# Kernel optimization log

Hardware: AMD Instinct MI355X
Metric: run time of the kernel (lower is better)

## Reference

```python
import jax, jax.numpy as jnp
import numpy as np

D_MODEL = 768
N_HEADS = 12
D_K = D_MODEL // N_HEADS
B, S = 2, 4096


def setup_inputs() -> dict:
    key = jax.random.key(0)
    ks = jax.random.split(key, 12)
    s_in = 1.0 / np.sqrt(D_MODEL)
    inp = {
        "Q": jax.random.normal(ks[0], (B, S, D_MODEL), jnp.float32),
        "K": jax.random.normal(ks[1], (B, S, D_MODEL), jnp.float32),
        "V": jax.random.normal(ks[2], (B, S, D_MODEL), jnp.float32),
        # nn.Linear weights are [out, in]; applied as x @ W.T + b
        "Wq": jax.random.normal(ks[3], (D_MODEL, D_MODEL), jnp.float32) * s_in,
        "bq": jax.random.normal(ks[4], (D_MODEL,), jnp.float32) * s_in,
        "Wk": jax.random.normal(ks[5], (D_MODEL, D_MODEL), jnp.float32) * s_in,
        "bk": jax.random.normal(ks[6], (D_MODEL,), jnp.float32) * s_in,
        "Wv": jax.random.normal(ks[7], (D_MODEL, D_MODEL), jnp.float32) * s_in,
        "bv": jax.random.normal(ks[8], (D_MODEL,), jnp.float32) * s_in,
        "Wo": jax.random.normal(ks[9], (D_MODEL, D_MODEL), jnp.float32) * s_in,
        "bo": jax.random.normal(ks[10], (D_MODEL,), jnp.float32) * s_in,
    }
    return inp


def _split_heads(x):
    b, s, _ = x.shape
    return x.reshape(b, s, N_HEADS, D_K).transpose(0, 2, 1, 3)  # [b,h,s,dk]


def reference(Q, K, V, Wq, bq, Wk, bk, Wv, bv, Wo, bo):
    q = _split_heads(Q @ Wq.T + bq)
    k = _split_heads(K @ Wk.T + bk)
    v = _split_heads(V @ Wv.T + bv)
    scale = 1.0 / np.sqrt(D_K).astype(np.float32)
    scores = jnp.einsum("bhqd,bhkd->bhqk", q, k) * scale  # [B,H,S,S]
    attn = jax.nn.softmax(scores, axis=-1)
    out = jnp.einsum("bhqk,bhkd->bhqd", attn, v)
    out = out.transpose(0, 2, 1, 3).reshape(Q.shape[0], Q.shape[1], D_MODEL)
    return out @ Wo.T + bo
```

## Files before the change

kernel.cpp:

```cpp
#include <hip/hip_runtime.h>
#include <hip/hip_bf16.h>

typedef __attribute__((ext_vector_type(8))) short short8;
typedef __attribute__((ext_vector_type(4))) float f32x4;
typedef __attribute__((ext_vector_type(4))) unsigned short ushort4v;

static __device__ __forceinline__ unsigned short f2bf(float f) {
  unsigned u = __float_as_uint(f);
  unsigned r = (u + 0x7fffu + ((u >> 16) & 1u)) >> 16;
  return (unsigned short)r;
}
static __device__ __forceinline__ short8 pack8(float4 a, float4 b) {
  short8 r;
  r[0] = (short)f2bf(a.x); r[1] = (short)f2bf(a.y);
  r[2] = (short)f2bf(a.z); r[3] = (short)f2bf(a.w);
  r[4] = (short)f2bf(b.x); r[5] = (short)f2bf(b.y);
  r[6] = (short)f2bf(b.z); r[7] = (short)f2bf(b.w);
  return r;
}

template <int CTRL>
static __device__ __forceinline__ float fmax_dpp(float x) {
  int t = __builtin_amdgcn_update_dpp(__float_as_int(x), __float_as_int(x),
                                      CTRL, 0xF, 0xF, true);
  return fmaxf(x, __int_as_float(t));
}
static __device__ __forceinline__ float max16_dpp(float x) {
  x = fmax_dpp<0xB1>(x);
  x = fmax_dpp<0x4E>(x);
  x = fmax_dpp<0x141>(x);
  x = fmax_dpp<0x140>(x);
  return x;
}

template<int XF32, int OUTF32>
__device__ __forceinline__ void gemm128(
    const void* Xp, const float* W, const float* bias,
    void* outp, float scale, int vt_mode, int bm, int bn)
{
  __shared__ unsigned short Als[128 * 32];
  __shared__ unsigned short Bls[128 * 32];

  const int tid = threadIdx.x;
  const int wave = tid >> 6, lane = tid & 63;
  const int g = lane >> 4, lo = lane & 15;
  const int wr = wave >> 1, wc = wave & 1;
  const int m0 = bm * 128, n0 = bn * 128;

  const f32x4 vzero = {0.f, 0.f, 0.f, 0.f};
  f32x4 acc[4][4];
#pragma unroll
  for (int m = 0; m < 4; ++m)
#pragma unroll
    for (int n = 0; n < 4; ++n) acc[m][n] = vzero;

  const int arow = tid >> 1;
  const int acol = (tid & 1) * 16;
  const float* Af = nullptr;
  const unsigned short* Ab = nullptr;
  if constexpr (XF32) Af = (const float*)Xp + (size_t)(m0 + arow) * 768 + acol;
  else                Ab = (const unsigned short*)Xp + (size_t)(m0 + arow) * 768 + acol;
  const float* Brow = W + (size_t)(n0 + arow) * 768 + acol;

  for (int k0 = 0; k0 < 768; k0 += 32) {
    short8 va0, va1;
    if constexpr (XF32) {
      float4 f0 = *(const float4*)(Af + k0);
      float4 f1 = *(const float4*)(Af + k0 + 4);
      float4 f2 = *(const float4*)(Af + k0 + 8);
      float4 f3 = *(const float4*)(Af + k0 + 12);
      va0 = pack8(f0, f1);
      va1 = pack8(f2, f3);
    } else {
      va0 = *(const short8*)(Ab + k0);
      va1 = *(const short8*)(Ab + k0 + 8);
    }
    float4 g0 = *(const float4*)(Brow + k0);
    float4 g1 = *(const float4*)(Brow + k0 + 4);
    float4 g2 = *(const float4*)(Brow + k0 + 8);
    float4 g3 = *(const float4*)(Brow + k0 + 12);
    short8 vb0 = pack8(g0, g1);
    short8 vb1 = pack8(g2, g3);

    __syncthreads();
    *(short8*)(Als + arow * 32 + acol)     = va0;
    *(short8*)(Als + arow * 32 + acol + 8) = va1;
    *(short8*)(Bls + arow * 32 + acol)     = vb0;
    *(short8*)(Bls + arow * 32 + acol + 8) = vb1;
    __syncthreads();

    short8 af[4], bf[4];
#pragma unroll
    for (int m = 0; m < 4; ++m)
      af[m] = *(const short8*)(Als + (wr * 64 + m * 16 + lo) * 32 + g * 8);
#pragma unroll
    for (int n = 0; n < 4; ++n)
      bf[n] = *(const short8*)(Bls + (wc * 64 + n * 16 + lo) * 32 + g * 8);
#pragma unroll
    for (int m = 0; m < 4; ++m)
#pragma unroll
      for (int n = 0; n < 4; ++n)
        acc[m][n] = __builtin_amdgcn_mfma_f32_16x16x32_bf16(af[m], bf[n], acc[m][n], 0, 0, 0);
  }

#pragma unroll
  for (int n = 0; n < 4; ++n) {
    const int ncol = n0 + wc * 64 + n * 16 + lo;
    const float bb = bias[ncol];
#pragma unroll
    for (int m = 0; m < 4; ++m) {
      const int rowb = m0 + wr * 64 + m * 16 + g * 4;
      if constexpr (OUTF32) {
        float* out = (float*)outp;
#pragma unroll
        for (int r = 0; r < 4; ++r)
          out[(size_t)(rowb + r) * 768 + ncol] = (acc[m][n][r] + bb) * scale;
      } else {
        unsigned short* out = (unsigned short*)outp;
        if (!vt_mode) {
#pragma unroll
          for (int r = 0; r < 4; ++r)
            out[(size_t)(rowb + r) * 768 + ncol] = f2bf((acc[m][n][r] + bb) * scale);
        } else {
          const int b = rowb >> 12, s = rowb & 4095;
          const int hh = ncol >> 6, d = ncol & 63;
          ushort4v pk;
#pragma unroll
          for (int r = 0; r < 4; ++r) pk[r] = f2bf((acc[m][n][r] + bb) * scale);
          *(ushort4v*)(out + (((size_t)b * 12 + hh) * 64 + d) * 4096 + s) = pk;
        }
      }
    }
  }
}

__global__ __launch_bounds__(256, 2) void qkv_proj(
    const float* __restrict__ Qi, const float* __restrict__ Ki,
    const float* __restrict__ Vi,
    const float* __restrict__ Wq, const float* __restrict__ bq,
    const float* __restrict__ Wk, const float* __restrict__ bk,
    const float* __restrict__ Wv, const float* __restrict__ bv,
    unsigned short* __restrict__ qo, unsigned short* __restrict__ ko,
    unsigned short* __restrict__ vto)
{
  const int z = blockIdx.z;
  const float* X = (z == 0) ? Qi : (z == 1) ? Ki : Vi;
  const float* W = (z == 0) ? Wq : (z == 1) ? Wk : Wv;
  const float* bb = (z == 0) ? bq : (z == 1) ? bk : bv;
  unsigned short* out = (z == 0) ? qo : (z == 1) ? ko : vto;
  const float scale = (z == 0) ? 0.18033688011f : 1.0f;
  gemm128<1, 0>(X, W, bb, out, scale, (z == 2) ? 1 : 0, blockIdx.x, blockIdx.y);
}

__global__ __launch_bounds__(256, 2) void out_proj(
    const unsigned short* __restrict__ X, const float* __restrict__ W,
    const float* __restrict__ bias, float* __restrict__ out)
{
  gemm128<0, 1>(X, W, bias, out, 1.0f, 0, blockIdx.x, blockIdx.y);
}

__global__ __launch_bounds__(512, 4) void attn_fwd(
    const unsigned short* qw, const unsigned short* __restrict__ kw,
    const unsigned short* __restrict__ vtw, unsigned short* ow)
{
  __shared__ char LDS[34816];

  const int tid = threadIdx.x, wave = tid >> 6, lane = tid & 63;
  const int g = lane >> 4, lo = lane & 15;
  const int bh = blockIdx.y, b = bh / 12, hh = bh % 12;
  const int q0 = blockIdx.x * 128 + wave * 16;

  short8 aq[2];
#pragma unroll
  for (int s = 0; s < 2; ++s)
    aq[s] = *(const short8*)(qw + (size_t)(b * 4096 + q0 + lo) * 768
                             + hh * 64 + s * 32 + g * 8);

  const f32x4 vzero = {0.f, 0.f, 0.f, 0.f};
  float mx[4];
  f32x4 lacc = vzero;
  f32x4 oacc[4];
#pragma unroll
  for (int r = 0; r < 4; ++r) mx[r] = -1e30f;
#pragma unroll
  for (int n = 0; n < 4; ++n) oacc[n] = vzero;

  short8 bone;
#pragma unroll
  for (int j = 0; j < 8; ++j) bone[j] = (short)0x3F80;

  const int rsw = (lo & 7) << 4;
  const int rb0 = lo * 128 + ((g * 16) ^ rsw);
  const int rb1 = lo * 128 + ((64 + g * 16) ^ rsw);
  char* const Kr0 = LDS + rb0;
  char* const Kr1 = LDS + rb1;
  char* const Vr0 = LDS + 8192 + rb0;
  char* const Vr1 = LDS + 8192 + rb1;
  char* const Pwr = LDS + 16384 + wave * 2304 + (g * 4) * 144 + lo * 2;
  char* const Prd = LDS + 16384 + wave * 2304 + lo * 144 + g * 16;

  const int srow = tid >> 3;
  const int sc = tid & 7;
  const unsigned short* krow = kw + ((size_t)b * 4096 + srow) * 768 + hh * 64 + sc * 8;
  const unsigned short* vrow = vtw + ((size_t)bh * 64 + srow) * 4096 + sc * 8;
  const int sdst = srow * 128 + ((sc * 16) ^ ((srow & 7) << 4));
  char* const Ksd = LDS + sdst;
  char* const Vsd = LDS + 8192 + sdst;

  short8 kl = *(const short8*)(krow);
  short8 vl = *(const short8*)(vrow);

  for (int kv0 = 0; kv0 < 4096; kv0 += 64) {
    asm volatile("s_waitcnt lgkmcnt(0)" ::: "memory");
    __builtin_amdgcn_s_barrier();
    *(short8*)Ksd = kl;
    *(short8*)Vsd = vl;
    if (kv0 + 64 < 4096) {
      kl = *(const short8*)(krow + (size_t)(kv0 + 64) * 768);
      vl = *(const short8*)(vrow + (kv0 + 64));
    }
    asm volatile("s_waitcnt lgkmcnt(0)" ::: "memory");
    __builtin_amdgcn_s_barrier();
    __builtin_amdgcn_sched_barrier(0);

    f32x4 sa[4];
#pragma unroll
    for (int n = 0; n < 4; ++n) {
      short8 bk0 = *(const short8*)(Kr0 + n * 2048);
      short8 bk1 = *(const short8*)(Kr1 + n * 2048);
      f32x4 t = vzero;
      t = __builtin_amdgcn_mfma_f32_16x16x32_bf16(aq[0], bk0, t, 0, 0, 0);
      t = __builtin_amdgcn_mfma_f32_16x16x32_bf16(aq[1], bk1, t, 0, 0, 0);
      sa[n] = t;
    }

#pragma unroll
    for (int r = 0; r < 4; ++r) {
      float pm = fmaxf(fmaxf(sa[0][r], sa[1][r]), fmaxf(sa[2][r], sa[3][r]));
      pm = max16_dpp(pm);
      if (pm > mx[r] + 8.f) {
        const float fr = __builtin_amdgcn_exp2f(mx[r] - pm);
        mx[r] = pm;
        lacc[r] *= fr;
#pragma unroll
        for (int nd = 0; nd < 4; ++nd) oacc[nd][r] *= fr;
      }
#pragma unroll
      for (int n = 0; n < 4; ++n) {
        const float pv = __builtin_amdgcn_exp2f(sa[n][r] - mx[r]);
        *(unsigned short*)(Pwr + r * 144 + n * 32) =
            (unsigned short)(__float_as_uint(pv) >> 16);
      }
    }

    short8 ap0 = *(const short8*)(Prd);
    short8 ap1 = *(const short8*)(Prd + 64);
#pragma unroll
    for (int nd = 0; nd < 4; ++nd) {
      short8 bv0 = *(const short8*)(Vr0 + nd * 2048);
      short8 bv1 = *(const short8*)(Vr1 + nd * 2048);
      oacc[nd] = __builtin_amdgcn_mfma_f32_16x16x32_bf16(ap0, bv0, oacc[nd], 0, 0, 0);
      oacc[nd] = __builtin_amdgcn_mfma_f32_16x16x32_bf16(ap1, bv1, oacc[nd], 0, 0, 0);
    }
    lacc = __builtin_amdgcn_mfma_f32_16x16x32_bf16(ap0, bone, lacc, 0, 0, 0);
    lacc = __builtin_amdgcn_mfma_f32_16x16x32_bf16(ap1, bone, lacc, 0, 0, 0);
  }

#pragma unroll
  for (int r = 0; r < 4; ++r) {
    const float inv = 1.f / lacc[r];
    const size_t rowoff = (size_t)(b * 4096 + q0 + g * 4 + r) * 768 + hh * 64;
#pragma unroll
    for (int nd = 0; nd < 4; ++nd)
      ow[rowoff + nd * 16 + lo] = f2bf(oacc[nd][r] * inv);
  }
}

extern "C" void kernel_launch(void* const* d_in, const int* in_sizes, int n_in,
                              void* d_out, int out_size, void* d_ws, size_t ws_size,
                              hipStream_t stream) {
  (void)in_sizes; (void)n_in; (void)out_size; (void)ws_size;
  const float* Qi = (const float*)d_in[0];
  const float* Ki = (const float*)d_in[1];
  const float* Vi = (const float*)d_in[2];
  const float* Wq = (const float*)d_in[3];
  const float* bq = (const float*)d_in[4];
  const float* Wk = (const float*)d_in[5];
  const float* bk = (const float*)d_in[6];
  const float* Wv = (const float*)d_in[7];
  const float* bv = (const float*)d_in[8];
  const float* Wo = (const float*)d_in[9];
  const float* bo = (const float*)d_in[10];

  unsigned short* ws = (unsigned short*)d_ws;
  const size_t NTOK = 8192u * 768u;
  unsigned short* qw  = ws;
  unsigned short* vtw = ws + NTOK;
  unsigned short* kwp = (unsigned short*)d_out;

  qkv_proj<<<dim3(64, 6, 3), 256, 0, stream>>>(Qi, Ki, Vi, Wq, bq, Wk, bk,
                                               Wv, bv, qw, kwp, vtw);
  attn_fwd<<<dim3(32, 24, 1), 512, 0, stream>>>(qw, kwp, vtw, qw);
  out_proj<<<dim3(64, 6, 1), 256, 0, stream>>>(qw, Wo, bo, (float*)d_out);
}
```

Baseline: 296.7 us.

## Double-buffer K/V tiles in LDS with one barrier per attention tile

The attention loop now keeps two K/V tile buffers in LDS. While the QK^T MFMAs run on one buffer, the next tile (already fetched into registers) is stored into the other, and loads for the tile after that are issued. This replaces two barriers per tile with one and lets global loads overlap more compute. In exchange it raises LDS use from about 34KB to 50KB per block, which may reduce occupancy, and past the end it issues clamped redundant loads of the last tile.

```diff
diff --git a/kernel.cpp b/kernel.cpp
--- a/kernel.cpp
+++ b/kernel.cpp
@@ -159,11 +159,69 @@
   gemm128<0, 1>(X, W, bias, out, 1.0f, 0, blockIdx.x, blockIdx.y);
 }
 
+#define ATTN_TILE(BO, KWR, VWR, KLD, VLD, TNEXT)                               \
+  {                                                                            \
+    asm volatile("s_waitcnt lgkmcnt(0)" ::: "memory");                         \
+    __builtin_amdgcn_s_barrier();                                              \
+    __builtin_amdgcn_sched_barrier(0);                                         \
+                                                    \
+    f32x4 sa[4];                                                               \
+    _Pragma("unroll")                                                          \
+    for (int n = 0; n < 4; ++n) {                                              \
+      short8 bk0 = *(const short8*)(Kr0 + (BO) + n * 2048);                    \
+      short8 bk1 = *(const short8*)(Kr1 + (BO) + n * 2048);                    \
+      f32x4 t = vzero;                                                         \
+      t = __builtin_amdgcn_mfma_f32_16x16x32_bf16(aq[0], bk0, t, 0, 0, 0);     \
+      t = __builtin_amdgcn_mfma_f32_16x16x32_bf16(aq[1], bk1, t, 0, 0, 0);     \
+      sa[n] = t;                                                               \
+    }                                                                          \
+             \
+    *(short8*)(Ksd + ((BO) ^ 8192)) = KWR;                                     \
+    *(short8*)(Vsd + ((BO) ^ 8192)) = VWR;                                     \
+    {                                                                          \
+      int tp = (TNEXT);                                                        \
+      if (tp > 63) tp = 63;                                                    \
+      KLD = *(const short8*)(krow + (size_t)(tp * 64) * 768);                  \
+      VLD = *(const short8*)(vrow + tp * 64);                                  \
+    }                                                                          \
+                                                 \
+    _Pragma("unroll")                                                          \
+    for (int r = 0; r < 4; ++r) {                                              \
+      float pm = fmaxf(fmaxf(sa[0][r], sa[1][r]), fmaxf(sa[2][r], sa[3][r]));  \
+      pm = max16_dpp(pm);                                                      \
+      if (pm > mx[r] + 8.f) {                                                  \
+        const float fr = __builtin_amdgcn_exp2f(mx[r] - pm);                   \
+        mx[r] = pm;                                                            \
+        lacc[r] *= fr;                                                         \
+        _Pragma("unroll")                                                      \
+        for (int nd = 0; nd < 4; ++nd) oacc[nd][r] *= fr;                      \
+      }                                                                        \
+      _Pragma("unroll")                                                        \
+      for (int n = 0; n < 4; ++n) {                                            \
+        const float pv = __builtin_amdgcn_exp2f(sa[n][r] - mx[r]);             \
+        *(unsigned short*)(Pwr + r * 144 + n * 32) =                           \
+            (unsigned short)(__float_as_uint(pv) >> 16);                       \
+      }                                                                        \
+    }                                                                          \
+                                        \
+    short8 ap0 = *(const short8*)(Prd);                                        \
+    short8 ap1 = *(const short8*)(Prd + 64);                                   \
+    _Pragma("unroll")                                                          \
+    for (int nd = 0; nd < 4; ++nd) {                                           \
+      short8 bv0 = *(const short8*)(Vr0 + (BO) + nd * 2048);                   \
+      short8 bv1 = *(const short8*)(Vr1 + (BO) + nd * 2048);                   \
+      oacc[nd] = __builtin_amdgcn_mfma_f32_16x16x32_bf16(ap0, bv0, oacc[nd], 0, 0, 0); \
+      oacc[nd] = __builtin_amdgcn_mfma_f32_16x16x32_bf16(ap1, bv1, oacc[nd], 0, 0, 0); \
+    }                                                                          \
+    lacc = __builtin_amdgcn_mfma_f32_16x16x32_bf16(ap0, bone, lacc, 0, 0, 0);  \
+    lacc = __builtin_amdgcn_mfma_f32_16x16x32_bf16(ap1, bone, lacc, 0, 0, 0);  \
+  }
+
 __global__ __launch_bounds__(512, 4) void attn_fwd(
     const unsigned short* qw, const unsigned short* __restrict__ kw,
     const unsigned short* __restrict__ vtw, unsigned short* ow)
 {
-  __shared__ char LDS[34816];
+  __shared__ char LDS[51200];
 
   const int tid = threadIdx.x, wave = tid >> 6, lane = tid & 63;
   const int g = lane >> 4, lo = lane & 15;
@@ -194,10 +252,10 @@
   const int rb1 = lo * 128 + ((64 + g * 16) ^ rsw);
   char* const Kr0 = LDS + rb0;
   char* const Kr1 = LDS + rb1;
-  char* const Vr0 = LDS + 8192 + rb0;
-  char* const Vr1 = LDS + 8192 + rb1;
-  char* const Pwr = LDS + 16384 + wave * 2304 + (g * 4) * 144 + lo * 2;
-  char* const Prd = LDS + 16384 + wave * 2304 + lo * 144 + g * 16;
+  char* const Vr0 = LDS + 16384 + rb0;
+  char* const Vr1 = LDS + 16384 + rb1;
+  char* const Pwr = LDS + 32768 + wave * 2304 + (g * 4) * 144 + lo * 2;
+  char* const Prd = LDS + 32768 + wave * 2304 + lo * 144 + g * 16;
 
   const int srow = tid >> 3;
   const int sc = tid & 7;
@@ -205,65 +263,21 @@
   const unsigned short* vrow = vtw + ((size_t)bh * 64 + srow) * 4096 + sc * 8;
   const int sdst = srow * 128 + ((sc * 16) ^ ((srow & 7) << 4));
   char* const Ksd = LDS + sdst;
-  char* const Vsd = LDS + 8192 + sdst;
-
-  short8 kl = *(const short8*)(krow);
-  short8 vl = *(const short8*)(vrow);
-
-  for (int kv0 = 0; kv0 < 4096; kv0 += 64) {
-    asm volatile("s_waitcnt lgkmcnt(0)" ::: "memory");
-    __builtin_amdgcn_s_barrier();
-    *(short8*)Ksd = kl;
-    *(short8*)Vsd = vl;
-    if (kv0 + 64 < 4096) {
-      kl = *(const short8*)(krow + (size_t)(kv0 + 64) * 768);
-      vl = *(const short8*)(vrow + (kv0 + 64));
-    }
-    asm volatile("s_waitcnt lgkmcnt(0)" ::: "memory");
-    __builtin_amdgcn_s_barrier();
-    __builtin_amdgcn_sched_barrier(0);
-
-    f32x4 sa[4];
-#pragma unroll
-    for (int n = 0; n < 4; ++n) {
-      short8 bk0 = *(const short8*)(Kr0 + n * 2048);
-      short8 bk1 = *(const short8*)(Kr1 + n * 2048);
-      f32x4 t = vzero;
-      t = __builtin_amdgcn_mfma_f32_16x16x32_bf16(aq[0], bk0, t, 0, 0, 0);
-      t = __builtin_amdgcn_mfma_f32_16x16x32_bf16(aq[1], bk1, t, 0, 0, 0);
-      sa[n] = t;
-    }
-
-#pragma unroll
-    for (int r = 0; r < 4; ++r) {
-      float pm = fmaxf(fmaxf(sa[0][r], sa[1][r]), fmaxf(sa[2][r], sa[3][r]));
-      pm = max16_dpp(pm);
-      if (pm > mx[r] + 8.f) {
-        const float fr = __builtin_amdgcn_exp2f(mx[r] - pm);
-        mx[r] = pm;
-        lacc[r] *= fr;
-#pragma unroll
-        for (int nd = 0; nd < 4; ++nd) oacc[nd][r] *= fr;
-      }
-#pragma unroll
-      for (int n = 0; n < 4; ++n) {
-        const float pv = __builtin_amdgcn_exp2f(sa[n][r] - mx[r]);
-        *(unsigned short*)(Pwr + r * 144 + n * 32) =
-            (unsigned short)(__float_as_uint(pv) >> 16);
-      }
-    }
-
-    short8 ap0 = *(const short8*)(Prd);
-    short8 ap1 = *(const short8*)(Prd + 64);
-#pragma unroll
-    for (int nd = 0; nd < 4; ++nd) {
-      short8 bv0 = *(const short8*)(Vr0 + nd * 2048);
-      short8 bv1 = *(const short8*)(Vr1 + nd * 2048);
-      oacc[nd] = __builtin_amdgcn_mfma_f32_16x16x32_bf16(ap0, bv0, oacc[nd], 0, 0, 0);
-      oacc[nd] = __builtin_amdgcn_mfma_f32_16x16x32_bf16(ap1, bv1, oacc[nd], 0, 0, 0);
-    }
-    lacc = __builtin_amdgcn_mfma_f32_16x16x32_bf16(ap0, bone, lacc, 0, 0, 0);
-    lacc = __builtin_amdgcn_mfma_f32_16x16x32_bf16(ap1, bone, lacc, 0, 0, 0);
+  char* const Vsd = LDS + 16384 + sdst;
+
+  {
+    short8 k0 = *(const short8*)(krow);
+    short8 v0 = *(const short8*)(vrow);
+    *(short8*)Ksd = k0;
+    *(short8*)Vsd = v0;
+  }
+  short8 klA = *(const short8*)(krow + (size_t)64 * 768);
+  short8 vlA = *(const short8*)(vrow + 64);
+  short8 klB, vlB;
+
+  for (int t = 0; t < 64; t += 2) {
+    ATTN_TILE(0,    klA, vlA, klB, vlB, t + 2)
+    ATTN_TILE(8192, klB, vlB, klA, vlA, t + 3)
   }
 
 #pragma unroll
```

New measurement: 294.6 us. About the same (-0.7%).

## Process two 16-row query tiles per wave in attention with 4-wave blocks

Applied to the files above, without the earlier changes.

Each wave in the attention kernel now handles 32 query rows (two 16-row MFMA tiles) instead of 16, so every K and V fragment read from LDS is reused across two tiles. Blocks shrink from 8 waves to 4 while still covering 128 queries, and each thread stages two 16-byte chunks per K/V tile instead of one. The aim is to halve LDS read traffic per unit of MFMA work and fewer barrier participants. In exchange, register pressure roughly doubles for accumulators and Q fragments, and there are fewer waves to hide latency.

```diff
diff --git a/kernel.cpp b/kernel.cpp
--- a/kernel.cpp
+++ b/kernel.cpp
@@ -159,7 +159,7 @@
   gemm128<0, 1>(X, W, bias, out, 1.0f, 0, blockIdx.x, blockIdx.y);
 }
 
-__global__ __launch_bounds__(512, 4) void attn_fwd(
+__global__ __launch_bounds__(256, 4) void attn_fwd(
     const unsigned short* qw, const unsigned short* __restrict__ kw,
     const unsigned short* __restrict__ vtw, unsigned short* ow)
 {
@@ -168,22 +168,28 @@
   const int tid = threadIdx.x, wave = tid >> 6, lane = tid & 63;
   const int g = lane >> 4, lo = lane & 15;
   const int bh = blockIdx.y, b = bh / 12, hh = bh % 12;
-  const int q0 = blockIdx.x * 128 + wave * 16;
-
-  short8 aq[2];
-#pragma unroll
-  for (int s = 0; s < 2; ++s)
-    aq[s] = *(const short8*)(qw + (size_t)(b * 4096 + q0 + lo) * 768
-                             + hh * 64 + s * 32 + g * 8);
+  const int q0 = blockIdx.x * 128 + wave * 32;
+
+  short8 aq[2][2];
+#pragma unroll
+  for (int m = 0; m < 2; ++m)
+#pragma unroll
+    for (int s = 0; s < 2; ++s)
+      aq[m][s] = *(const short8*)(qw + (size_t)(b * 4096 + q0 + m * 16 + lo) * 768
+                                  + hh * 64 + s * 32 + g * 8);
 
   const f32x4 vzero = {0.f, 0.f, 0.f, 0.f};
-  float mx[4];
-  f32x4 lacc = vzero;
-  f32x4 oacc[4];
-#pragma unroll
-  for (int r = 0; r < 4; ++r) mx[r] = -1e30f;
-#pragma unroll
-  for (int n = 0; n < 4; ++n) oacc[n] = vzero;
+  float mx[2][4];
+  f32x4 lacc[2];
+  f32x4 oacc[2][4];
+#pragma unroll
+  for (int m = 0; m < 2; ++m) {
+    lacc[m] = vzero;
+#pragma unroll
+    for (int r = 0; r < 4; ++r) mx[m][r] = -1e30f;
+#pragma unroll
+    for (int n = 0; n < 4; ++n) oacc[m][n] = vzero;
+  }
 
   short8 bone;
 #pragma unroll
@@ -196,84 +202,108 @@
   char* const Kr1 = LDS + rb1;
   char* const Vr0 = LDS + 8192 + rb0;
   char* const Vr1 = LDS + 8192 + rb1;
-  char* const Pwr = LDS + 16384 + wave * 2304 + (g * 4) * 144 + lo * 2;
-  char* const Prd = LDS + 16384 + wave * 2304 + lo * 144 + g * 16;
-
-  const int srow = tid >> 3;
-  const int sc = tid & 7;
+  char* const Pwr = LDS + 16384 + wave * 4608 + (g * 4) * 144 + lo * 2;
+  char* const Prd = LDS + 16384 + wave * 4608 + lo * 144 + g * 16;
+
+  const int srow = tid >> 2;
+  const int sc = (tid & 3) * 2;
   const unsigned short* krow = kw + ((size_t)b * 4096 + srow) * 768 + hh * 64 + sc * 8;
   const unsigned short* vrow = vtw + ((size_t)bh * 64 + srow) * 4096 + sc * 8;
-  const int sdst = srow * 128 + ((sc * 16) ^ ((srow & 7) << 4));
-  char* const Ksd = LDS + sdst;
-  char* const Vsd = LDS + 8192 + sdst;
-
-  short8 kl = *(const short8*)(krow);
-  short8 vl = *(const short8*)(vrow);
+  const int sd0 = srow * 128 + ((sc * 16) ^ ((srow & 7) << 4));
+  const int sd1 = sd0 ^ 16;
+  char* const Ksd0 = LDS + sd0;
+  char* const Ksd1 = LDS + sd1;
+  char* const Vsd0 = LDS + 8192 + sd0;
+  char* const Vsd1 = LDS + 8192 + sd1;
+
+  short8 kl0 = *(const short8*)(krow);
+  short8 kl1 = *(const short8*)(krow + 8);
+  short8 vl0 = *(const short8*)(vrow);
+  short8 vl1 = *(const short8*)(vrow + 8);
 
   for (int kv0 = 0; kv0 < 4096; kv0 += 64) {
     asm volatile("s_waitcnt lgkmcnt(0)" ::: "memory");
     __builtin_amdgcn_s_barrier();
-    *(short8*)Ksd = kl;
-    *(short8*)Vsd = vl;
+    *(short8*)Ksd0 = kl0;
+    *(short8*)Ksd1 = kl1;
+    *(short8*)Vsd0 = vl0;
+    *(short8*)Vsd1 = vl1;
     if (kv0 + 64 < 4096) {
-      kl = *(const short8*)(krow + (size_t)(kv0 + 64) * 768);
-      vl = *(const short8*)(vrow + (kv0 + 64));
+      kl0 = *(const short8*)(krow + (size_t)(kv0 + 64) * 768);
+      kl1 = *(const short8*)(krow + (size_t)(kv0 + 64) * 768 + 8);
+      vl0 = *(const short8*)(vrow + kv0 + 64);
+      vl1 = *(const short8*)(vrow + kv0 + 64 + 8);
     }
     asm volatile("s_waitcnt lgkmcnt(0)" ::: "memory");
     __builtin_amdgcn_s_barrier();
     __builtin_amdgcn_sched_barrier(0);
 
-    f32x4 sa[4];
-#pragma unroll
-    for (int n = 0; n < 4; ++n) {
-      short8 bk0 = *(const short8*)(Kr0 + n * 2048);
-      short8 bk1 = *(const short8*)(Kr1 + n * 2048);
-      f32x4 t = vzero;
-      t = __builtin_amdgcn_mfma_f32_16x16x32_bf16(aq[0], bk0, t, 0, 0, 0);
-      t = __builtin_amdgcn_mfma_f32_16x16x32_bf16(aq[1], bk1, t, 0, 0, 0);
-      sa[n] = t;
-    }
-
-#pragma unroll
-    for (int r = 0; r < 4; ++r) {
-      float pm = fmaxf(fmaxf(sa[0][r], sa[1][r]), fmaxf(sa[2][r], sa[3][r]));
-      pm = max16_dpp(pm);
-      if (pm > mx[r] + 8.f) {
-        const float fr = __builtin_amdgcn_exp2f(mx[r] - pm);
-        mx[r] = pm;
-        lacc[r] *= fr;
-#pragma unroll
-        for (int nd = 0; nd < 4; ++nd) oacc[nd][r] *= fr;
+#pragma unroll
+    for (int m = 0; m < 2; ++m) {
+      f32x4 sa[4];
+#pragma unroll
+      for (int n = 0; n < 4; ++n) {
+        short8 bk0 = *(const short8*)(Kr0 + n * 2048);
+        short8 bk1 = *(const short8*)(Kr1 + n * 2048);
+        f32x4 t = vzero;
+        t = __builtin_amdgcn_mfma_f32_16x16x32_bf16(aq[m][0], bk0, t, 0, 0, 0);
+        t = __builtin_amdgcn_mfma_f32_16x16x32_bf16(aq[m][1], bk1, t, 0, 0, 0);
+        sa[n] = t;
       }
 #pragma unroll
-      for (int n = 0; n < 4; ++n) {
-        const float pv = __builtin_amdgcn_exp2f(sa[n][r] - mx[r]);
-        *(unsigned short*)(Pwr + r * 144 + n * 32) =
-            (unsigned short)(__float_as_uint(pv) >> 16);
+      for (int r = 0; r < 4; ++r) {
+        float pm = fmaxf(fmaxf(sa[0][r], sa[1][r]), fmaxf(sa[2][r], sa[3][r]));
+        pm = max16_dpp(pm);
+        if (pm > mx[m][r] + 8.f) {
+          const float fr = __builtin_amdgcn_exp2f(mx[m][r] - pm);
+          mx[m][r] = pm;
+          lacc[m][r] *= fr;
+#pragma unroll
+          for (int nd = 0; nd < 4; ++nd) oacc[m][nd][r] *= fr;
+        }
+#pragma unroll
+        for (int n = 0; n < 4; ++n) {
+          const float pv = __builtin_amdgcn_exp2f(sa[n][r] - mx[m][r]);
+          *(unsigned short*)(Pwr + m * 2304 + r * 144 + n * 32) =
+              (unsigned short)(__float_as_uint(pv) >> 16);
+        }
       }
     }
 
-    short8 ap0 = *(const short8*)(Prd);
-    short8 ap1 = *(const short8*)(Prd + 64);
+    short8 ap[2][2];
+#pragma unroll
+    for (int m = 0; m < 2; ++m) {
+      ap[m][0] = *(const short8*)(Prd + m * 2304);
+      ap[m][1] = *(const short8*)(Prd + m * 2304 + 64);
+    }
 #pragma unroll
     for (int nd = 0; nd < 4; ++nd) {
       short8 bv0 = *(const short8*)(Vr0 + nd * 2048);
       short8 bv1 = *(const short8*)(Vr1 + nd * 2048);
-      oacc[nd] = __builtin_amdgcn_mfma_f32_16x16x32_bf16(ap0, bv0, oacc[nd], 0, 0, 0);
-      oacc[nd] = __builtin_amdgcn_mfma_f32_16x16x32_bf16(ap1, bv1, oacc[nd], 0, 0, 0);
-    }
-    lacc = __builtin_amdgcn_mfma_f32_16x16x32_bf16(ap0, bone, lacc, 0, 0, 0);
-    lacc = __builtin_amdgcn_mfma_f32_16x16x32_bf16(ap1, bone, lacc, 0, 0, 0);
+#pragma unroll
+      for (int m = 0; m < 2; ++m) {
+        oacc[m][nd] = __builtin_amdgcn_mfma_f32_16x16x32_bf16(ap[m][0], bv0, oacc[m][nd], 0, 0, 0);
+        oacc[m][nd] = __builtin_amdgcn_mfma_f32_16x16x32_bf16(ap[m][1], bv1, oacc[m][nd], 0, 0, 0);
+      }
+    }
+#pragma unroll
+    for (int m = 0; m < 2; ++m) {
+      lacc[m] = __builtin_amdgcn_mfma_f32_16x16x32_bf16(ap[m][0], bone, lacc[m], 0, 0, 0);
+      lacc[m] = __builtin_amdgcn_mfma_f32_16x16x32_bf16(ap[m][1], bone, lacc[m], 0, 0, 0);
+    }
   }
 
 #pragma unroll
-  for (int r = 0; r < 4; ++r) {
-    const float inv = 1.f / lacc[r];
-    const size_t rowoff = (size_t)(b * 4096 + q0 + g * 4 + r) * 768 + hh * 64;
-#pragma unroll
-    for (int nd = 0; nd < 4; ++nd)
-      ow[rowoff + nd * 16 + lo] = f2bf(oacc[nd][r] * inv);
-  }
+  for (int m = 0; m < 2; ++m)
+#pragma unroll
+    for (int r = 0; r < 4; ++r) {
+      const float inv = 1.f / lacc[m][r];
+      const size_t rowoff =
+          (size_t)(b * 4096 + q0 + m * 16 + g * 4 + r) * 768 + hh * 64;
+#pragma unroll
+      for (int nd = 0; nd < 4; ++nd)
+        ow[rowoff + nd * 16 + lo] = f2bf(oacc[m][nd][r] * inv);
+    }
 }
 
 extern "C" void kernel_launch(void* const* d_in, const int* in_sizes, int n_in,
@@ -300,6 +330,6 @@
 
   qkv_proj<<<dim3(64, 6, 3), 256, 0, stream>>>(Qi, Ki, Vi, Wq, bq, Wk, bk,
                                                Wv, bv, qw, kwp, vtw);
-  attn_fwd<<<dim3(32, 24, 1), 512, 0, stream>>>(qw, kwp, vtw, qw);
+  attn_fwd<<<dim3(32, 24, 1), 256, 0, stream>>>(qw, kwp, vtw, qw);
   out_proj<<<dim3(64, 6, 1), 256, 0, stream>>>(qw, Wo, bo, (float*)d_out);
 }
```

New measurement: 353.7 us. 1.19x slower.
